# Optimization experiments

Hardware: AMD Instinct MI355X
Metric: run time of the kernel (lower is better)

Reference implementation:

```python
import jax, jax.numpy as jnp
import numpy as np
import math

B, S, E, H, L, VOCAB, OUT = 32, 1024, 512, 8, 2, 20000, 1
D = E // H


def positional_encoding(seq_length, embed_size):
    position = jnp.arange(seq_length, dtype=jnp.float32)[:, None]
    div_term = jnp.exp(jnp.arange(0, embed_size, 2, dtype=jnp.float32) * (-math.log(10000.0) / embed_size))
    pe = jnp.zeros((seq_length, embed_size), dtype=jnp.float32)
    pe = pe.at[:, 0::2].set(jnp.sin(position * div_term))
    pe = pe.at[:, 1::2].set(jnp.cos(position * div_term))
    return pe


def setup_inputs() -> dict:
    key = jax.random.key(0)
    ks = jax.random.split(key, 12)
    inputs = jax.random.randint(ks[0], (B, S), 0, VOCAB)
    s = 1.0 / math.sqrt(E)
    embed_table = jax.random.normal(ks[1], (VOCAB, E), jnp.float32)
    embed_table = embed_table.at[0].set(0.0)  # padding_idx=0
    # per-layer Q,K,V,O linear weights [L,E,E] (applied as x @ W + b) and biases [L,E]
    Wq = jax.random.normal(ks[2], (L, E, E), jnp.float32) * s
    Wk = jax.random.normal(ks[3], (L, E, E), jnp.float32) * s
    Wv = jax.random.normal(ks[4], (L, E, E), jnp.float32) * s
    Wo = jax.random.normal(ks[5], (L, E, E), jnp.float32) * s
    bq = jax.random.normal(ks[6], (L, E), jnp.float32) * s
    bk = jax.random.normal(ks[7], (L, E), jnp.float32) * s
    bv = jax.random.normal(ks[8], (L, E), jnp.float32) * s
    bo = jax.random.normal(ks[9], (L, E), jnp.float32) * s
    W_out = jax.random.normal(ks[10], (E, OUT), jnp.float32) * s
    b_out = jax.random.normal(ks[11], (OUT,), jnp.float32) * s
    return {"inputs": inputs, "embed_table": embed_table, "Wq": Wq, "bq": bq,
            "Wk": Wk, "bk": bk, "Wv": Wv, "bv": bv, "Wo": Wo, "bo": bo,
            "W_out": W_out, "b_out": b_out}


def _mha(x, Wq, bq, Wk, bk, Wv, bv, Wo, bo, mask):
    b, s = x.shape[:2]
    def heads(W, bias):
        return (x @ W + bias).reshape(b, s, H, D).transpose(0, 2, 1, 3)  # [b,H,s,D]
    q, k, v = heads(Wq, bq), heads(Wk, bk), heads(Wv, bv)
    scores = jnp.einsum('bhqd,bhkd->bhqk', q, k) / math.sqrt(D)
    scores = jnp.where(mask, -1e9, scores)
    prob = jax.nn.softmax(scores, axis=-1)
    out = jnp.einsum('bhqk,bhkd->bhqd', prob, v)
    out = out.transpose(0, 2, 1, 3).reshape(b, s, E)
    return out @ Wo + bo


def reference(inputs, embed_table, Wq, bq, Wk, bk, Wv, bv, Wo, bo, W_out, b_out):
    embeds = embed_table[inputs]  # [B,S,E]
    embeds = embeds + positional_encoding(inputs.shape[1], embeds.shape[-1])
    mask = jnp.triu(jnp.ones((inputs.shape[1], inputs.shape[1]), bool), k=1)  # future mask
    out = embeds
    for l in range(L):
        attn = _mha(out, Wq[l], bq[l], Wk[l], bk[l], Wv[l], bv[l], Wo[l], bo[l], mask)
        out = out + jax.nn.relu(attn)  # dropout is identity (eval / p=0)
    return out @ W_out + b_out
```

## Files before the change

### kernel.cpp

```cpp
#include <hip/hip_runtime.h>

typedef unsigned short u16;
typedef unsigned int u32;
using short8  = __attribute__((ext_vector_type(8))) short;
using floatx4 = __attribute__((ext_vector_type(4))) float;

#define NB 32
#define SEQ 1024
#define EMB 512
#define NH 8
#define HD 64
#define NLAYER 2
#define M_ROWS (NB * SEQ)

__device__ __forceinline__ float bf2f(u16 u) {
  union { u32 i; float f; } v; v.i = ((u32)u) << 16; return v.f;
}
__device__ __forceinline__ u16 f2bf(float f) {
  union { float f; u32 i; } v; v.f = f;
  u32 r = v.i + 0x7fffu + ((v.i >> 16) & 1u);
  return (u16)(r >> 16);
}

#if __has_builtin(__builtin_amdgcn_exp2f)
#define EXP2F __builtin_amdgcn_exp2f
#else
#define EXP2F exp2f
#endif

typedef __attribute__((address_space(3))) unsigned int lds_u32_t;
typedef __attribute__((address_space(1))) const unsigned int gbl_u32_t;
__device__ __forceinline__ void gload16(void* lds, const void* g) {
  gbl_u32_t* gp = (gbl_u32_t*)(unsigned long long)g;
  lds_u32_t* lp = (lds_u32_t*)(unsigned int)(unsigned long long)lds;
  __builtin_amdgcn_global_load_lds(gp, lp, 16, 0, 0);
}

__global__ void prep_weights(const float* __restrict__ Wq, const float* __restrict__ Wk,
                             const float* __restrict__ Wv, const float* __restrict__ Wo,
                             u16* __restrict__ WtQKV, u16* __restrict__ WtO) {
  int idx = blockIdx.x * 256 + threadIdx.x;
  const int QKV_TOT = NLAYER * 3 * EMB * EMB;
  if (idx < QKV_TOT) {
    int l = idx / (3 * EMB * EMB);
    int rem = idx % (3 * EMB * EMB);
    int n = rem / EMB, kk = rem % EMB;
    int w = n >> 9, e = n & 511;
    const float* src = (w == 0) ? Wq : (w == 1) ? Wk : Wv;
    WtQKV[idx] = f2bf(src[((size_t)l * EMB + kk) * EMB + e]);
  } else {
    int j = idx - QKV_TOT;
    int l = j / (EMB * EMB);
    int rem = j % (EMB * EMB);
    int n = rem / EMB, kk = rem % EMB;
    WtO[j] = f2bf(Wo[((size_t)l * EMB + kk) * EMB + n]);
  }
}

__global__ void embed_pe(const int* __restrict__ inp, const float* __restrict__ table,
                         u16* __restrict__ x) {
  int row = blockIdx.x;
  int tok = inp[row];
  int s = row & (SEQ - 1);
  const float negln = -9.210340371976184f / (float)EMB;
  for (int e = threadIdx.x; e < EMB; e += blockDim.x) {
    float val = table[(size_t)tok * EMB + e];
    int i = e >> 1;
    float dt = __expf((float)(2 * i) * negln);
    float ang = (float)s * dt;
    float pe = (e & 1) ? __cosf(ang) : __sinf(ang);
    x[(size_t)row * EMB + e] = f2bf(val + pe);
  }
}

#define BK 32

__global__ __launch_bounds__(256) void gemm_bt(
    const u16* __restrict__ A, const u16* __restrict__ Bt, int K, int mode,
    const float* bias0, const float* bias1, const float* bias2,
    u16* out0, u16* out1, u16* out2, const u16* resid, int Nstride) {
  __shared__ u16 sA[2][128][BK];
  __shared__ u16 sB[2][128][BK];
  int tid = threadIdx.x;
  int wave = tid >> 6, lane = tid & 63;
  int quad = lane >> 4, l16 = lane & 15;
  int wm = wave >> 1, wn = wave & 1;

  int NT = (mode == 0) ? 12 : 4;
  int blk = blockIdx.x;
  int xcd = blk & 7, slot = blk >> 3;
  int mtl = slot / NT, ntl = slot % NT;
  int bm0 = (xcd * 32 + mtl) * 128;
  int bn0 = ntl * 128;
  bool vswap = (mode == 0) && (bn0 >= 1024);

  floatx4 acc[4][4];
#pragma unroll
  for (int i = 0; i < 4; ++i)
#pragma unroll
    for (int j = 0; j < 4; ++j) acc[i][j] = (floatx4){0.f, 0.f, 0.f, 0.f};

  int rb = wave * 32;
  int lrow = lane >> 2;
  int gcg = ((lane & 3) ^ ((lane >> 3) & 3)) * 8;
  int rsl = (quad ^ ((l16 >> 1) & 3)) * 8;

  const u16* Arow0 = &A[(size_t)(bm0 + rb + lrow) * K + gcg];
  const u16* Arow1 = &A[(size_t)(bm0 + rb + 16 + lrow) * K + gcg];
  const u16* Brow0 = &Bt[(size_t)(bn0 + rb + lrow) * K + gcg];
  const u16* Brow1 = &Bt[(size_t)(bn0 + rb + 16 + lrow) * K + gcg];

  gload16(&sA[0][rb][0],      Arow0);
  gload16(&sA[0][rb + 16][0], Arow1);
  gload16(&sB[0][rb][0],      Brow0);
  gload16(&sB[0][rb + 16][0], Brow1);

  const int niter = K / BK;
  int ibuf = 0;
  for (int it = 0; it < niter; ++it) {
    if (it + 1 < niter) {
      int k1 = (it + 1) * BK;
      int nb = ibuf ^ 1;
      gload16(&sA[nb][rb][0],      Arow0 + k1);
      gload16(&sA[nb][rb + 16][0], Arow1 + k1);
      gload16(&sB[nb][rb][0],      Brow0 + k1);
      gload16(&sB[nb][rb + 16][0], Brow1 + k1);
      asm volatile("s_waitcnt vmcnt(4)" ::: "memory");
    } else {
      asm volatile("s_waitcnt vmcnt(0)" ::: "memory");
    }
    asm volatile("s_barrier" ::: "memory");

    short8 af[4], bfr[4];
#pragma unroll
    for (int mi = 0; mi < 4; ++mi)
      af[mi] = *(const short8*)&sA[ibuf][wm * 64 + mi * 16 + l16][rsl];
#pragma unroll
    for (int ni = 0; ni < 4; ++ni)
      bfr[ni] = *(const short8*)&sB[ibuf][wn * 64 + ni * 16 + l16][rsl];
    if (!vswap) {
#pragma unroll
      for (int mi = 0; mi < 4; ++mi)
#pragma unroll
        for (int ni = 0; ni < 4; ++ni)
          acc[mi][ni] = __builtin_amdgcn_mfma_f32_16x16x32_bf16(af[mi], bfr[ni], acc[mi][ni], 0, 0, 0);
    } else {
#pragma unroll
      for (int mi = 0; mi < 4; ++mi)
#pragma unroll
        for (int ni = 0; ni < 4; ++ni)
          acc[mi][ni] = __builtin_amdgcn_mfma_f32_16x16x32_bf16(bfr[ni], af[mi], acc[mi][ni], 0, 0, 0);
    }
    asm volatile("s_waitcnt lgkmcnt(0)" ::: "memory");
    asm volatile("s_barrier" ::: "memory");
    ibuf ^= 1;
  }

  u16* scr = ((u16*)sA) + wave * (16 * 68);
  int erow = lane >> 5;
  int dcol = lane & 31;

  if (!vswap) {
    int w = bn0 >> 9;
    const float* bp = (mode == 1) ? bias0 : ((w == 0) ? bias0 : bias1);
    float sc = (mode == 0 && w == 0) ? 0.18033688011112042f : 1.0f;
    float bv[4];
#pragma unroll
    for (int ni = 0; ni < 4; ++ni)
      bv[ni] = bp[(bn0 + wn * 64 + ni * 16 + l16) & 511];

#pragma unroll
    for (int mi = 0; mi < 4; ++mi) {
#pragma unroll
      for (int ni = 0; ni < 4; ++ni)
#pragma unroll
        for (int r = 0; r < 4; ++r) {
          float t = (acc[mi][ni][r] + bv[ni]) * sc;
          if (mode == 1) t = fmaxf(t, 0.f);
          scr[(quad * 4 + r) * 68 + ni * 16 + l16] = f2bf(t);
        }
      asm volatile("s_waitcnt lgkmcnt(0)" ::: "memory");

      int m0 = bm0 + wm * 64 + mi * 16;
      int colg = bn0 + wn * 64 + dcol * 2;
#pragma unroll
      for (int p = 0; p < 8; ++p) {
        int row = p * 2 + erow;
        u32 d2 = *(const u32*)&scr[row * 68 + dcol * 2];
        int m = m0 + row;
        if (mode == 0) {
          int e = colg & 511, h = e >> 6, d = e & 63;
          int b = m >> 10, sid = m & 1023;
          u16* optr = (w == 0) ? out0 : out1;
          *(u32*)&optr[((size_t)(b * NH + h) * SEQ + sid) * HD + d] = d2;
        } else {
          size_t off = (size_t)m * Nstride + colg;
          u32 rs = *(const u32*)&resid[off];
          float lo = bf2f((u16)d2) + bf2f((u16)rs);
          float hi = bf2f((u16)(d2 >> 16)) + bf2f((u16)(rs >> 16));
          *(u32*)&out0[off] = ((u32)f2bf(hi) << 16) | f2bf(lo);
        }
      }
      asm volatile("s_waitcnt lgkmcnt(0)" ::: "memory");
    }
  } else {
    float bvv[4][4];
#pragma unroll
    for (int ni = 0; ni < 4; ++ni)
#pragma unroll
      for (int r = 0; r < 4; ++r)
        bvv[ni][r] = bias2[(bn0 + wn * 64 + ni * 16 + quad * 4 + r) & 511];

    int b = (bm0 + wm * 64) >> 10;
    int sid0 = (bm0 + wm * 64) & 1023;
    int n0 = bn0 + wn * 64;
    int h = (n0 >> 6) & 7;
#pragma unroll
    for (int ni = 0; ni < 4; ++ni) {
#pragma unroll
      for (int mi = 0; mi < 4; ++mi)
#pragma unroll
        for (int r = 0; r < 4; ++r)
          scr[(quad * 4 + r) * 68 + mi * 16 + l16] = f2bf(acc[mi][ni][r] + bvv[ni][r]);
      asm volatile("s_waitcnt lgkmcnt(0)" ::: "memory");

      int d0 = (n0 & 63) + ni * 16;
#pragma unroll
      for (int p = 0; p < 8; ++p) {
        int row = p * 2 + erow;
        u32 d2 = *(const u32*)&scr[row * 68 + dcol * 2];
        *(u32*)&out2[((size_t)(b * NH + h) * HD + d0 + row) * SEQ + sid0 + dcol * 2] = d2;
      }
      asm volatile("s_waitcnt lgkmcnt(0)" ::: "memory");
    }
  }
}

__device__ __forceinline__ void stage_tile64(u16 (*dst)[64], const u16* g, int gstride,
                                             int wave, int lane) {
  int r = lane >> 3;
  int gcg = ((lane & 7) ^ r) * 8;
#pragma unroll
  for (int c = 0; c < 2; ++c) {
    int row0 = (wave * 2 + c) * 8;
    gload16(&dst[row0][0], &g[(size_t)(row0 + r) * gstride + gcg]);
  }
}
#define RD8(T, row, cg) (*(const short8*)&T[row][(((cg) ^ ((row) & 7)) * 8)])

__global__ __launch_bounds__(256) void attn_kernel(
    const u16* __restrict__ q, const u16* __restrict__ k, const u16* __restrict__ vt,
    u16* __restrict__ o) {
  int blk = blockIdx.x;
  int xcd = blk & 7, slot = blk >> 3;
  int bh = xcd * 32 + (slot >> 3);
  int qtp = slot & 7;
  int b = bh >> 3, h = bh & 7;
  int qA0 = qtp * 128, qB0 = qA0 + 64;
  __shared__ u16 sQ[128][64], sK[64][64], sV[64][64];
  __shared__ u16 sP[2][64][68];
  int tid = threadIdx.x, wave = tid >> 6, lane = tid & 63;
  int quad = lane >> 4, l16 = lane & 15;

  stage_tile64((u16(*)[64])&sQ[0][0],  &q[((size_t)bh * SEQ + qA0) * HD], HD, wave, lane);
  stage_tile64((u16(*)[64])&sQ[64][0], &q[((size_t)bh * SEQ + qB0) * HD], HD, wave, lane);

  short8 ones;
#pragma unroll
  for (int j = 0; j < 8; ++j) ones[j] = (short)0x3F80;

  floatx4 accoA[4], accoB[4], accsumA, accsumB;
#pragma unroll
  for (int i = 0; i < 4; ++i) {
    accoA[i] = (floatx4){0.f, 0.f, 0.f, 0.f};
    accoB[i] = (floatx4){0.f, 0.f, 0.f, 0.f};
  }
  accsumA = (floatx4){0.f, 0.f, 0.f, 0.f};
  accsumB = (floatx4){0.f, 0.f, 0.f, 0.f};
  short8 aqA0 = {}, aqA1 = {}, aqB0 = {}, aqB1 = {};

  auto process = [&](short8 aq0, short8 aq1, int qX0, bool diag, int sub,
                     floatx4* acco, floatx4& accsum, int k0) {
    floatx4 accs[4];
#pragma unroll
    for (int i = 0; i < 4; ++i) accs[i] = (floatx4){0.f, 0.f, 0.f, 0.f};
#pragma unroll
    for (int nt = 0; nt < 4; ++nt) {
      int rbk = nt * 16 + l16;
      accs[nt] = __builtin_amdgcn_mfma_f32_16x16x32_bf16(aq0, RD8(sK, rbk, quad), accs[nt], 0, 0, 0);
      accs[nt] = __builtin_amdgcn_mfma_f32_16x16x32_bf16(aq1, RD8(sK, rbk, 4 + quad), accs[nt], 0, 0, 0);
    }
    int prow = wave * 16 + quad * 4;
    if (!diag) {
#pragma unroll
      for (int nt = 0; nt < 4; ++nt)
#pragma unroll
        for (int r = 0; r < 4; ++r) {
          float p = EXP2F(fminf(accs[nt][r], 108.f));
          sP[sub][prow + r][nt * 16 + l16] = (u16)(__float_as_uint(p) >> 16);
        }
    } else {
      int qg_base = qX0 + prow;
#pragma unroll
      for (int nt = 0; nt < 4; ++nt) {
        int kg = k0 + nt * 16 + l16;
#pragma unroll
        for (int r = 0; r < 4; ++r) {
          float p = EXP2F(fminf(accs[nt][r], 108.f));
          if (kg > qg_base + r) p = 0.f;
          sP[sub][prow + r][nt * 16 + l16] = (u16)(__float_as_uint(p) >> 16);
        }
      }
    }
    asm volatile("s_waitcnt lgkmcnt(0)" ::: "memory");
#pragma unroll
    for (int cst = 0; cst < 2; ++cst) {
      short8 ap = *(const short8*)&sP[sub][wave * 16 + l16][cst * 32 + quad * 8];
#pragma unroll
      for (int dt = 0; dt < 4; ++dt) {
        int rv = dt * 16 + l16;
        acco[dt] = __builtin_amdgcn_mfma_f32_16x16x32_bf16(ap, RD8(sV, rv, cst * 4 + quad), acco[dt], 0, 0, 0);
      }
      accsum = __builtin_amdgcn_mfma_f32_16x16x32_bf16(ap, ones, accsum, 0, 0, 0);
    }
  };

  int ktmax = 2 * qtp + 1;
  for (int kt = 0; kt <= ktmax; ++kt) {
    int k0 = kt * 64;
    __syncthreads();
    stage_tile64(sK, &k[((size_t)bh * SEQ + k0) * HD], HD, wave, lane);
    stage_tile64(sV, &vt[(size_t)bh * HD * SEQ + k0], SEQ, wave, lane);
    __syncthreads();

    if (kt == 0) {
      int ra = wave * 16 + l16;
      aqA0 = RD8(sQ, ra, quad);
      aqA1 = RD8(sQ, ra, 4 + quad);
      int rb_ = 64 + wave * 16 + l16;
      aqB0 = RD8(sQ, rb_, quad);
      aqB1 = RD8(sQ, rb_, 4 + quad);
    }

    if (kt <= 2 * qtp)
      process(aqA0, aqA1, qA0, kt == 2 * qtp, 0, accoA, accsumA, k0);
    process(aqB0, aqB1, qB0, kt == ktmax, 1, accoB, accsumB, k0);
  }

#pragma unroll
  for (int dt = 0; dt < 4; ++dt)
#pragma unroll
    for (int r = 0; r < 4; ++r) {
      int rowoff = wave * 16 + quad * 4 + r;
      int col = h * HD + dt * 16 + l16;
      o[((size_t)b * SEQ + qA0 + rowoff) * EMB + col] = f2bf(accoA[dt][r] / accsumA[r]);
      o[((size_t)b * SEQ + qB0 + rowoff) * EMB + col] = f2bf(accoB[dt][r] / accsumB[r]);
    }
}

__global__ __launch_bounds__(256) void out_proj(const u16* __restrict__ x,
                                                const float* __restrict__ wout,
                                                const float* __restrict__ bout,
                                                float* __restrict__ out) {
  int wave = threadIdx.x >> 6, lane = threadIdx.x & 63;
  int m = blockIdx.x * 4 + wave;
  union { uint4 vv; u16 s[8]; } xv;
  xv.vv = *(const uint4*)&x[(size_t)m * EMB + lane * 8];
  float4 w0 = *(const float4*)&wout[lane * 8];
  float4 w1 = *(const float4*)&wout[lane * 8 + 4];
  float wv[8] = {w0.x, w0.y, w0.z, w0.w, w1.x, w1.y, w1.z, w1.w};
  float s = 0.f;
#pragma unroll
  for (int j = 0; j < 8; ++j) s += bf2f(xv.s[j]) * wv[j];
#pragma unroll
  for (int sh = 1; sh < 64; sh <<= 1) s += __shfl_xor(s, sh, 64);
  if (lane == 0) out[m] = s + bout[0];
}

extern "C" void kernel_launch(void* const* d_in, const int* in_sizes, int n_in,
                              void* d_out, int out_size, void* d_ws, size_t ws_size,
                              hipStream_t stream) {
  const int*   inp   = (const int*)d_in[0];
  const float* table = (const float*)d_in[1];
  const float* Wq    = (const float*)d_in[2];
  const float* bq    = (const float*)d_in[3];
  const float* Wk    = (const float*)d_in[4];
  const float* bk    = (const float*)d_in[5];
  const float* Wv    = (const float*)d_in[6];
  const float* bv    = (const float*)d_in[7];
  const float* Wo    = (const float*)d_in[8];
  const float* bo    = (const float*)d_in[9];
  const float* Wout  = (const float*)d_in[10];
  const float* bout  = (const float*)d_in[11];
  float* outp = (float*)d_out;

  char* ws = (char*)d_ws;
  const size_t SZ = (size_t)M_ROWS * EMB * 2;
  u16* x      = (u16*)(ws);
  u16* qb     = (u16*)(ws + SZ);
  u16* kb     = (u16*)(ws + 2 * SZ);
  u16* vb     = (u16*)(ws + 3 * SZ);
  u16* attn_b = (u16*)(ws + 4 * SZ);
  u16* WtQKV  = (u16*)(ws + 5 * SZ);
  u16* WtO    = (u16*)(ws + 5 * SZ + (size_t)NLAYER * 3 * EMB * EMB * 2);

  prep_weights<<<8192, 256, 0, stream>>>(Wq, Wk, Wv, Wo, WtQKV, WtO);
  embed_pe<<<M_ROWS, 256, 0, stream>>>(inp, table, x);

  for (int l = 0; l < NLAYER; ++l) {
    gemm_bt<<<3072, 256, 0, stream>>>(
        x, WtQKV + (size_t)l * 3 * EMB * EMB, EMB, 0,
        bq + l * EMB, bk + l * EMB, bv + l * EMB, qb, kb, vb, nullptr, 0);
    attn_kernel<<<2048, 256, 0, stream>>>(qb, kb, vb, attn_b);
    gemm_bt<<<1024, 256, 0, stream>>>(
        attn_b, WtO + (size_t)l * EMB * EMB, EMB, 1,
        bo + l * EMB, nullptr, nullptr, x, nullptr, nullptr, x, EMB);
  }
  out_proj<<<8192, 256, 0, stream>>>(x, Wout, bout, outp);
}
```

Baseline: 615.7 us.

## Triple-buffer GEMM LDS staging and pack bf16 conversions in epilogue

Raises the GEMM's LDS staging from double to triple buffering, prefetching two K-slices ahead with adjusted vmcnt waits so global loads overlap longer with MFMA work. The epilogue now uses the hardware v_cvt_pk_bf16_f32 instruction in place of software rounding, folds the bias and scale into a single fma, and hoists address arithmetic out of the store loops. The extra buffer increases LDS use per block, which may lower occupancy.

```diff
diff --git a/kernel.cpp b/kernel.cpp
--- a/kernel.cpp
+++ b/kernel.cpp
@@ -20,6 +20,11 @@
   union { float f; u32 i; } v; v.f = f;
   u32 r = v.i + 0x7fffu + ((v.i >> 16) & 1u);
   return (u16)(r >> 16);
+}
+__device__ __forceinline__ u32 cvtpk(float a, float b) {
+  u32 r;
+  asm volatile("v_cvt_pk_bf16_f32 %0, %1, %2" : "=v"(r) : "v"(a), "v"(b));
+  return r;
 }
 
 #if __has_builtin(__builtin_amdgcn_exp2f)
@@ -79,8 +84,8 @@
     const u16* __restrict__ A, const u16* __restrict__ Bt, int K, int mode,
     const float* bias0, const float* bias1, const float* bias2,
     u16* out0, u16* out1, u16* out2, const u16* resid, int Nstride) {
-  __shared__ u16 sA[2][128][BK];
-  __shared__ u16 sB[2][128][BK];
+  __shared__ u16 sA[3][128][BK];
+  __shared__ u16 sB[3][128][BK];
   int tid = threadIdx.x;
   int wave = tid >> 6, lane = tid & 63;
   int quad = lane >> 4, l16 = lane & 15;
@@ -114,17 +119,22 @@
   gload16(&sA[0][rb + 16][0], Arow1);
   gload16(&sB[0][rb][0],      Brow0);
   gload16(&sB[0][rb + 16][0], Brow1);
+  gload16(&sA[1][rb][0],      Arow0 + BK);
+  gload16(&sA[1][rb + 16][0], Arow1 + BK);
+  gload16(&sB[1][rb][0],      Brow0 + BK);
+  gload16(&sB[1][rb + 16][0], Brow1 + BK);
 
   const int niter = K / BK;
-  int ibuf = 0;
+  int c0 = 0, c1 = 1, c2 = 2;
   for (int it = 0; it < niter; ++it) {
-    if (it + 1 < niter) {
-      int k1 = (it + 1) * BK;
-      int nb = ibuf ^ 1;
-      gload16(&sA[nb][rb][0],      Arow0 + k1);
-      gload16(&sA[nb][rb + 16][0], Arow1 + k1);
-      gload16(&sB[nb][rb][0],      Brow0 + k1);
-      gload16(&sB[nb][rb + 16][0], Brow1 + k1);
+    if (it + 2 < niter) {
+      int k2 = (it + 2) * BK;
+      gload16(&sA[c2][rb][0],      Arow0 + k2);
+      gload16(&sA[c2][rb + 16][0], Arow1 + k2);
+      gload16(&sB[c2][rb][0],      Brow0 + k2);
+      gload16(&sB[c2][rb + 16][0], Brow1 + k2);
+      asm volatile("s_waitcnt vmcnt(8)" ::: "memory");
+    } else if (it + 1 < niter) {
       asm volatile("s_waitcnt vmcnt(4)" ::: "memory");
     } else {
       asm volatile("s_waitcnt vmcnt(0)" ::: "memory");
@@ -134,10 +144,10 @@
     short8 af[4], bfr[4];
 #pragma unroll
     for (int mi = 0; mi < 4; ++mi)
-      af[mi] = *(const short8*)&sA[ibuf][wm * 64 + mi * 16 + l16][rsl];
+      af[mi] = *(const short8*)&sA[c0][wm * 64 + mi * 16 + l16][rsl];
 #pragma unroll
     for (int ni = 0; ni < 4; ++ni)
-      bfr[ni] = *(const short8*)&sB[ibuf][wn * 64 + ni * 16 + l16][rsl];
+      bfr[ni] = *(const short8*)&sB[c0][wn * 64 + ni * 16 + l16][rsl];
     if (!vswap) {
 #pragma unroll
       for (int mi = 0; mi < 4; ++mi)
@@ -153,7 +163,7 @@
     }
     asm volatile("s_waitcnt lgkmcnt(0)" ::: "memory");
     asm volatile("s_barrier" ::: "memory");
-    ibuf ^= 1;
+    int t = c0; c0 = c1; c1 = c2; c2 = t;
   }
 
   u16* scr = ((u16*)sA) + wave * (16 * 68);
@@ -164,41 +174,57 @@
     int w = bn0 >> 9;
     const float* bp = (mode == 1) ? bias0 : ((w == 0) ? bias0 : bias1);
     float sc = (mode == 0 && w == 0) ? 0.18033688011112042f : 1.0f;
-    float bv[4];
+    float bvs[4];
 #pragma unroll
     for (int ni = 0; ni < 4; ++ni)
-      bv[ni] = bp[(bn0 + wn * 64 + ni * 16 + l16) & 511];
-
+      bvs[ni] = bp[(bn0 + wn * 64 + ni * 16 + l16) & 511] * sc;
+
+    int colg = bn0 + wn * 64 + dcol * 2;
 #pragma unroll
     for (int mi = 0; mi < 4; ++mi) {
 #pragma unroll
-      for (int ni = 0; ni < 4; ++ni)
-#pragma unroll
-        for (int r = 0; r < 4; ++r) {
-          float t = (acc[mi][ni][r] + bv[ni]) * sc;
-          if (mode == 1) t = fmaxf(t, 0.f);
-          scr[(quad * 4 + r) * 68 + ni * 16 + l16] = f2bf(t);
+      for (int ni = 0; ni < 4; ++ni) {
+        float t0 = fmaf(acc[mi][ni][0], sc, bvs[ni]);
+        float t1 = fmaf(acc[mi][ni][1], sc, bvs[ni]);
+        float t2 = fmaf(acc[mi][ni][2], sc, bvs[ni]);
+        float t3 = fmaf(acc[mi][ni][3], sc, bvs[ni]);
+        if (mode == 1) {
+          t0 = fmaxf(t0, 0.f); t1 = fmaxf(t1, 0.f);
+          t2 = fmaxf(t2, 0.f); t3 = fmaxf(t3, 0.f);
         }
+        u32 p01 = cvtpk(t0, t1), p23 = cvtpk(t2, t3);
+        int base = (quad * 4) * 68 + ni * 16 + l16;
+        scr[base]       = (u16)p01;
+        scr[base + 68]  = (u16)(p01 >> 16);
+        scr[base + 136] = (u16)p23;
+        scr[base + 204] = (u16)(p23 >> 16);
+      }
       asm volatile("s_waitcnt lgkmcnt(0)" ::: "memory");
 
       int m0 = bm0 + wm * 64 + mi * 16;
-      int colg = bn0 + wn * 64 + dcol * 2;
-#pragma unroll
-      for (int p = 0; p < 8; ++p) {
-        int row = p * 2 + erow;
-        u32 d2 = *(const u32*)&scr[row * 68 + dcol * 2];
-        int m = m0 + row;
-        if (mode == 0) {
-          int e = colg & 511, h = e >> 6, d = e & 63;
-          int b = m >> 10, sid = m & 1023;
-          u16* optr = (w == 0) ? out0 : out1;
-          *(u32*)&optr[((size_t)(b * NH + h) * SEQ + sid) * HD + d] = d2;
-        } else {
-          size_t off = (size_t)m * Nstride + colg;
-          u32 rs = *(const u32*)&resid[off];
+      if (mode == 0) {
+        int e = colg & 511, hh = e >> 6, dd = e & 63;
+        int bb = m0 >> 10, sid0 = m0 & 1023;
+        u16* optr = (w == 0) ? out0 : out1;
+        u16* op = &optr[((size_t)(bb * NH + hh) * SEQ + sid0) * HD + dd];
+#pragma unroll
+        for (int p = 0; p < 8; ++p) {
+          int row = p * 2 + erow;
+          u32 d2 = *(const u32*)&scr[row * 68 + dcol * 2];
+          *(u32*)&op[(size_t)row * HD] = d2;
+        }
+      } else {
+        size_t off0 = (size_t)m0 * Nstride + colg;
+        const u16* rp = &resid[off0];
+        u16* wp = &out0[off0];
+#pragma unroll
+        for (int p = 0; p < 8; ++p) {
+          int row = p * 2 + erow;
+          u32 d2 = *(const u32*)&scr[row * 68 + dcol * 2];
+          u32 rs = *(const u32*)&rp[(size_t)row * Nstride];
           float lo = bf2f((u16)d2) + bf2f((u16)rs);
           float hi = bf2f((u16)(d2 >> 16)) + bf2f((u16)(rs >> 16));
-          *(u32*)&out0[off] = ((u32)f2bf(hi) << 16) | f2bf(lo);
+          *(u32*)&wp[(size_t)row * Nstride] = cvtpk(lo, hi);
         }
       }
       asm volatile("s_waitcnt lgkmcnt(0)" ::: "memory");
@@ -218,18 +244,27 @@
 #pragma unroll
     for (int ni = 0; ni < 4; ++ni) {
 #pragma unroll
-      for (int mi = 0; mi < 4; ++mi)
-#pragma unroll
-        for (int r = 0; r < 4; ++r)
-          scr[(quad * 4 + r) * 68 + mi * 16 + l16] = f2bf(acc[mi][ni][r] + bvv[ni][r]);
+      for (int mi = 0; mi < 4; ++mi) {
+        float t0 = acc[mi][ni][0] + bvv[ni][0];
+        float t1 = acc[mi][ni][1] + bvv[ni][1];
+        float t2 = acc[mi][ni][2] + bvv[ni][2];
+        float t3 = acc[mi][ni][3] + bvv[ni][3];
+        u32 p01 = cvtpk(t0, t1), p23 = cvtpk(t2, t3);
+        int base = (quad * 4) * 68 + mi * 16 + l16;
+        scr[base]       = (u16)p01;
+        scr[base + 68]  = (u16)(p01 >> 16);
+        scr[base + 136] = (u16)p23;
+        scr[base + 204] = (u16)(p23 >> 16);
+      }
       asm volatile("s_waitcnt lgkmcnt(0)" ::: "memory");
 
       int d0 = (n0 & 63) + ni * 16;
+      u16* op2 = &out2[((size_t)(b * NH + h) * HD + d0) * SEQ + sid0 + dcol * 2];
 #pragma unroll
       for (int p = 0; p < 8; ++p) {
         int row = p * 2 + erow;
         u32 d2 = *(const u32*)&scr[row * 68 + dcol * 2];
-        *(u32*)&out2[((size_t)(b * NH + h) * HD + d0 + row) * SEQ + sid0 + dcol * 2] = d2;
+        *(u32*)&op2[(size_t)row * SEQ] = d2;
       }
       asm volatile("s_waitcnt lgkmcnt(0)" ::: "memory");
     }
```

Measured after the change: 598.2 us. 1.03x faster.
